# Performance work log

Hardware: AMD Instinct MI355X
Metric: run time of the kernel (lower is better)

## Reference

```python
import jax, jax.numpy as jnp
import numpy as np


def setup_inputs() -> dict:
    key = jax.random.key(0)
    k0, k1, k2, k3 = jax.random.split(key, 4)
    B, S, D, E = 8, 4096, 1024, 3
    tokens = jax.random.normal(k0, (B, S, D), dtype=jnp.float32)
    # nn.Linear weights are [out_features, in_features]; kaiming-uniform-like scale
    scale = 1.0 / np.sqrt(D)
    Wq = jax.random.uniform(k1, (E, D), jnp.float32, -scale, scale)
    Wk = jax.random.uniform(k2, (E, D), jnp.float32, -scale, scale)
    Wv = jax.random.uniform(k3, (E, D), jnp.float32, -scale, scale)
    return {"tokens": tokens, "Wq": Wq, "Wk": Wk, "Wv": Wv}


def reference(tokens, Wq, Wk, Wv):
    # q, k, v: [B, S, E]   (E = num_experts = 3)
    q = jnp.einsum("bsd,ed->bse", tokens, Wq)
    k = jnp.einsum("bsd,ed->bse", tokens, Wk)
    v = jnp.einsum("bsd,ed->bse", tokens, Wv)
    # outer product attention: [B, S, E, E]
    attn = q[..., :, None] * k[..., None, :]
    attn = jax.nn.softmax(attn, axis=-1)
    # attn @ v: [B, S, E]
    logits = jnp.einsum("bsef,bsf->bse", attn, v)
    weights = jax.nn.softmax(logits, axis=-1)
    return weights
```

## Files before the change

kernel.cpp:

```cpp
#include <hip/hip_runtime.h>

typedef float f4 __attribute__((ext_vector_type(4)));

#define TPW 8

template <int CTRL>
__device__ __forceinline__ float dpp_add(float x) {
  int yi = __builtin_amdgcn_update_dpp(0, __float_as_int(x), CTRL, 0xF, 0xF, true);
  return x + __int_as_float(yi);
}

__device__ __forceinline__ float wave_sum63(float x) {
  x = dpp_add<0x111>(x);
  x = dpp_add<0x112>(x);
  x = dpp_add<0x114>(x);
  x = dpp_add<0x118>(x);
  x = dpp_add<0x142>(x);
  x = dpp_add<0x143>(x);
  return x;
}

__device__ __forceinline__ void softmax3(const float* s9, float& o0, float& o1, float& o2) {
  float lg[3];
#pragma unroll
  for (int e = 0; e < 3; ++e) {
    float e0 = __expf(s9[e] * s9[3]);
    float e1 = __expf(s9[e] * s9[4]);
    float e2 = __expf(s9[e] * s9[5]);
    float den = (e0 + e1) + e2;
    float num = e0 * s9[6] + e1 * s9[7] + e2 * s9[8];
    lg[e] = num * __builtin_amdgcn_rcpf(den);
  }
  float u0 = __expf(lg[0]);
  float u1 = __expf(lg[1]);
  float u2 = __expf(lg[2]);
  float rs = __builtin_amdgcn_rcpf((u0 + u1) + u2);
  o0 = u0 * rs; o1 = u1 * rs; o2 = u2 * rs;
}

__global__ __launch_bounds__(256, 2)
void moa_kernel(const float* __restrict__ tok,
                const float* __restrict__ Wq,
                const float* __restrict__ Wk,
                const float* __restrict__ Wv,
                float* __restrict__ out,
                int n_tokens) {
  const int lane = threadIdx.x & 63;
  const int wid  = (blockIdx.x << 2) | (threadIdx.x >> 6);
  const int base = lane << 2;

  f4 w[9][4];
  const float* Wp[3] = {Wq, Wk, Wv};
#pragma unroll
  for (int m = 0; m < 3; ++m)
#pragma unroll
    for (int e = 0; e < 3; ++e)
#pragma unroll
      for (int c = 0; c < 4; ++c)
        w[m * 3 + e][c] = *(const f4*)(Wp[m] + e * 1024 + c * 256 + base);

  const int t0 = wid * TPW;
  if (t0 >= n_tokens) return;
  const float* wbase = tok + (size_t)t0 * 1024 + base;

  f4 xa[2][4], xb[2][4];
#pragma unroll
  for (int p = 0; p < 2; ++p)
#pragma unroll
    for (int c = 0; c < 4; ++c)
      xa[p][c] = *(const f4*)(wbase + (size_t)p * 1024 + c * 256);

  float outv = 0.0f;

#pragma unroll
  for (int i = 0; i < TPW / 2; ++i) {
    f4 (&cur)[2][4] = (i & 1) ? xb : xa;
    f4 (&nxt)[2][4] = (i & 1) ? xa : xb;

    if (i < TPW / 2 - 1) {
#pragma unroll
      for (int p = 0; p < 2; ++p)
#pragma unroll
        for (int c = 0; c < 4; ++c)
          nxt[p][c] = *(const f4*)(wbase + (size_t)(2 * (i + 1) + p) * 1024 + c * 256);
    }

    float sA[9], sB[9];
#pragma unroll
    for (int j = 0; j < 9; ++j) {
      f4 a = cur[0][0] * w[j][0];
      a += cur[0][1] * w[j][1];
      a += cur[0][2] * w[j][2];
      a += cur[0][3] * w[j][3];
      sA[j] = (a.x + a.y) + (a.z + a.w);
      f4 b = cur[1][0] * w[j][0];
      b += cur[1][1] * w[j][1];
      b += cur[1][2] * w[j][2];
      b += cur[1][3] * w[j][3];
      sB[j] = (b.x + b.y) + (b.z + b.w);
    }

#pragma unroll
    for (int j = 0; j < 9; ++j) {
      sA[j] = wave_sum63(sA[j]);
      sB[j] = wave_sum63(sB[j]);
    }

    float a0, a1, a2, b0, b1, b2;
    softmax3(sA, a0, a1, a2);
    softmax3(sB, b0, b1, b2);

    float rA[3] = {
      __int_as_float(__builtin_amdgcn_readlane(__float_as_int(a0), 63)),
      __int_as_float(__builtin_amdgcn_readlane(__float_as_int(a1), 63)),
      __int_as_float(__builtin_amdgcn_readlane(__float_as_int(a2), 63))};
    float rB[3] = {
      __int_as_float(__builtin_amdgcn_readlane(__float_as_int(b0), 63)),
      __int_as_float(__builtin_amdgcn_readlane(__float_as_int(b1), 63)),
      __int_as_float(__builtin_amdgcn_readlane(__float_as_int(b2), 63))};

#pragma unroll
    for (int c = 0; c < 3; ++c) {
      outv = (lane == 6 * i + c)     ? rA[c] : outv;
      outv = (lane == 6 * i + 3 + c) ? rB[c] : outv;
    }
  }

  const int oidx = t0 * 3 + lane;
  if (lane < 3 * TPW) out[oidx] = outv;
}

extern "C" void kernel_launch(void* const* d_in, const int* in_sizes, int n_in,
                              void* d_out, int out_size, void* d_ws, size_t ws_size,
                              hipStream_t stream) {
  const float* tok = (const float*)d_in[0];
  const float* Wq  = (const float*)d_in[1];
  const float* Wk  = (const float*)d_in[2];
  const float* Wv  = (const float*)d_in[3];
  float* out = (float*)d_out;

  const int n_tokens = in_sizes[0] / 1024;
  const int waves    = (n_tokens + TPW - 1) / TPW;
  const int blocks   = (waves + 3) / 4;

  hipLaunchKernelGGL(moa_kernel, dim3(blocks), dim3(256), 0, stream,
                     tok, Wq, Wk, Wv, out, n_tokens);
}
```

Before: 27.65 us.

## Stage weights in LDS and defer per-token softmax to one lane each

Each block now cooperatively copies the 9x1024 weight rows into shared memory once and waves read their register slices from LDS instead of global memory. Per-token reduced dot products are gathered into per-lane registers via readlane, and the two-stage softmax runs once at the end on lanes 0..7, each handling one token. This removes the redundant softmax computation every lane did per token pair. The bounds check and round-up grid sizing are dropped, so token counts not divisible by 32 would be handled incorrectly, and it adds 36KB LDS per block plus a barrier.

```diff
diff --git a/kernel.cpp b/kernel.cpp
--- a/kernel.cpp
+++ b/kernel.cpp
@@ -20,47 +20,40 @@
   return x;
 }
 
-__device__ __forceinline__ void softmax3(const float* s9, float& o0, float& o1, float& o2) {
-  float lg[3];
-#pragma unroll
-  for (int e = 0; e < 3; ++e) {
-    float e0 = __expf(s9[e] * s9[3]);
-    float e1 = __expf(s9[e] * s9[4]);
-    float e2 = __expf(s9[e] * s9[5]);
-    float den = (e0 + e1) + e2;
-    float num = e0 * s9[6] + e1 * s9[7] + e2 * s9[8];
-    lg[e] = num * __builtin_amdgcn_rcpf(den);
-  }
-  float u0 = __expf(lg[0]);
-  float u1 = __expf(lg[1]);
-  float u2 = __expf(lg[2]);
-  float rs = __builtin_amdgcn_rcpf((u0 + u1) + u2);
-  o0 = u0 * rs; o1 = u1 * rs; o2 = u2 * rs;
-}
-
 __global__ __launch_bounds__(256, 2)
 void moa_kernel(const float* __restrict__ tok,
                 const float* __restrict__ Wq,
                 const float* __restrict__ Wk,
                 const float* __restrict__ Wv,
-                float* __restrict__ out,
-                int n_tokens) {
-  const int lane = threadIdx.x & 63;
-  const int wid  = (blockIdx.x << 2) | (threadIdx.x >> 6);
+                float* __restrict__ out) {
+  __shared__ __align__(16) float wlds[9 * 1024];
+  const int tid = threadIdx.x;
+
+  {
+    const float* Wsrc[3] = {Wq, Wk, Wv};
+#pragma unroll
+    for (int r = 0; r < 9; ++r) {
+      const int idx = r * 256 + tid;
+      const int j   = idx >> 8;
+      const int k4  = idx & 255;
+      *(f4*)(wlds + j * 1024 + k4 * 4) =
+          *(const f4*)(Wsrc[j / 3] + (j % 3) * 1024 + k4 * 4);
+    }
+  }
+  __syncthreads();
+
+  const int lane = tid & 63;
+  const int wid  = (blockIdx.x << 2) | (tid >> 6);
   const int base = lane << 2;
 
   f4 w[9][4];
-  const float* Wp[3] = {Wq, Wk, Wv};
 #pragma unroll
-  for (int m = 0; m < 3; ++m)
+  for (int j = 0; j < 9; ++j)
 #pragma unroll
-    for (int e = 0; e < 3; ++e)
-#pragma unroll
-      for (int c = 0; c < 4; ++c)
-        w[m * 3 + e][c] = *(const f4*)(Wp[m] + e * 1024 + c * 256 + base);
+    for (int c = 0; c < 4; ++c)
+      w[j][c] = *(const f4*)(wlds + j * 1024 + c * 256 + base);
 
   const int t0 = wid * TPW;
-  if (t0 >= n_tokens) return;
   const float* wbase = tok + (size_t)t0 * 1024 + base;
 
   f4 xa[2][4], xb[2][4];
@@ -70,7 +63,9 @@
     for (int c = 0; c < 4; ++c)
       xa[p][c] = *(const f4*)(wbase + (size_t)p * 1024 + c * 256);
 
-  float outv = 0.0f;
+  float dst[9];
+#pragma unroll
+  for (int j = 0; j < 9; ++j) dst[j] = 0.0f;
 
 #pragma unroll
   for (int i = 0; i < TPW / 2; ++i) {
@@ -106,28 +101,38 @@
       sB[j] = wave_sum63(sB[j]);
     }
 
-    float a0, a1, a2, b0, b1, b2;
-    softmax3(sA, a0, a1, a2);
-    softmax3(sB, b0, b1, b2);
-
-    float rA[3] = {
-      __int_as_float(__builtin_amdgcn_readlane(__float_as_int(a0), 63)),
-      __int_as_float(__builtin_amdgcn_readlane(__float_as_int(a1), 63)),
-      __int_as_float(__builtin_amdgcn_readlane(__float_as_int(a2), 63))};
-    float rB[3] = {
-      __int_as_float(__builtin_amdgcn_readlane(__float_as_int(b0), 63)),
-      __int_as_float(__builtin_amdgcn_readlane(__float_as_int(b1), 63)),
-      __int_as_float(__builtin_amdgcn_readlane(__float_as_int(b2), 63))};
-
 #pragma unroll
-    for (int c = 0; c < 3; ++c) {
-      outv = (lane == 6 * i + c)     ? rA[c] : outv;
-      outv = (lane == 6 * i + 3 + c) ? rB[c] : outv;
+    for (int j = 0; j < 9; ++j) {
+      float a63 = __int_as_float(__builtin_amdgcn_readlane(__float_as_int(sA[j]), 63));
+      float b63 = __int_as_float(__builtin_amdgcn_readlane(__float_as_int(sB[j]), 63));
+      dst[j] = (lane == 2 * i)     ? a63 : dst[j];
+      dst[j] = (lane == 2 * i + 1) ? b63 : dst[j];
     }
   }
 
-  const int oidx = t0 * 3 + lane;
-  if (lane < 3 * TPW) out[oidx] = outv;
+  if (lane < TPW) {
+    float r[9];
+#pragma unroll
+    for (int j = 0; j < 9; ++j) r[j] = dst[j];
+    float lg[3];
+#pragma unroll
+    for (int e = 0; e < 3; ++e) {
+      float e0 = __expf(r[e] * r[3]);
+      float e1 = __expf(r[e] * r[4]);
+      float e2 = __expf(r[e] * r[5]);
+      float den = (e0 + e1) + e2;
+      float num = e0 * r[6] + e1 * r[7] + e2 * r[8];
+      lg[e] = num * __builtin_amdgcn_rcpf(den);
+    }
+    float u0 = __expf(lg[0]);
+    float u1 = __expf(lg[1]);
+    float u2 = __expf(lg[2]);
+    float rs = __builtin_amdgcn_rcpf((u0 + u1) + u2);
+    float* op = out + (size_t)(t0 + lane) * 3;
+    op[0] = u0 * rs;
+    op[1] = u1 * rs;
+    op[2] = u2 * rs;
+  }
 }
 
 extern "C" void kernel_launch(void* const* d_in, const int* in_sizes, int n_in,
@@ -140,9 +145,9 @@
   float* out = (float*)d_out;
 
   const int n_tokens = in_sizes[0] / 1024;
-  const int waves    = (n_tokens + TPW - 1) / TPW;
-  const int blocks   = (waves + 3) / 4;
+  const int waves    = n_tokens / TPW;
+  const int blocks   = waves / 4;
 
   hipLaunchKernelGGL(moa_kernel, dim3(blocks), dim3(256), 0, stream,
-                     tok, Wq, Wk, Wv, out, n_tokens);
+                     tok, Wq, Wk, Wv, out);
 }
```

Measured after the change: 33.97 us. 22.9% more time.
